# Performance work log

Hardware: AMD Instinct MI355X
Metric: run time of the kernel (lower is better)

Reference implementation:

```python
import jax, jax.numpy as jnp
import numpy as np

B, C, L = 2048, 9605, 8
ALPHA = 0.5        # self.alpha
ALPHA1 = 0.05      # margin
ALPHA2 = 2.0       # asymmetric scale when violated
ALPHA3 = 5.0       # logistic sharpness
ALPHA_OTHER = 0.3  # floor on top-k threshold
TOPK = 16          # x_sorted[15] -> 16th largest


def setup_inputs() -> dict:
    key = jax.random.key(0)
    k1, k2, k3, k4 = jax.random.split(key, 4)
    x = jax.random.normal(k1, (B, C), dtype=jnp.float32)
    # each class assigned to one of 5*L slots; slots < L are whitelist groups,
    # the rest are 'other' classes (like total_indices in the torch code)
    gid = jax.random.randint(k4, (C,), 0, 5 * L)
    gid = gid.at[:L].set(jnp.arange(L))  # guarantee every group is non-empty
    group_mask = gid[None, :] == jnp.arange(L)[:, None]  # [L, C] bool
    # sparse multi-label binarized targets (~14 positives/sample)
    y = (jax.random.uniform(k2, (B, C)) < 0.0015).astype(jnp.float32)
    y_neg = (jax.random.uniform(k3, (B, C)) < 0.0015).astype(jnp.float32)
    return {"x": x, "y": y, "y_neg": y_neg, "group_mask": group_mask}


def _rank_loss(x1, x2):
    # our_rank_loss: sigmoid(alpha3*(x2-x1+margin)), scaled by alpha2 when violated
    d = x2 - x1 + ALPHA1
    s = jax.nn.sigmoid(ALPHA3 * d)
    return jnp.where(d > 0, ALPHA2 * s, s)


def reference(x, y, y_neg, group_mask):
    xs = jax.nn.sigmoid(x)  # [B, C]
    # top_k_thres = max(16th-largest sigmoid score, alpha_other)
    thres = jnp.maximum(jax.lax.top_k(xs, TOPK)[0][:, TOPK - 1], ALPHA_OTHER)  # [B]
    maskf = group_mask.astype(xs.dtype)  # [L, C]
    neg_inf = jnp.array(-jnp.inf, xs.dtype)
    # per-sample max score inside each whitelist group: [B, L]
    group_max = jnp.max(jnp.where(group_mask[None, :, :], xs[:, None, :], neg_inf), axis=-1)
    # find_gt_whitelist: group is 'hit' if any positive target inside it
    gt = (y @ maskf.T) > 0        # [B, L]
    gt_neg = (y_neg @ maskf.T) > 0  # [B, L]
    has_gt = jnp.any(gt, axis=-1)    # [B]; False <=> sentinel len(all_labels)
    has_neg = jnp.any(gt_neg, axis=-1)
    # ---- case B: sample hits at least one whitelist group ----
    rl_correct = _rank_loss(group_max, thres[:, None])    # gt groups above thres
    rl_incorrect = _rank_loss(thres[:, None], group_max)  # non-gt groups below thres
    caseB = jnp.sum(jnp.where(gt, rl_correct, rl_incorrect), axis=-1)  # [B]
    # ---- case A: no whitelist group hit ----
    union = jnp.any(group_mask, axis=0)  # [C] union of all whitelist classes
    union_max = jnp.max(jnp.where(union[None, :], xs, neg_inf), axis=-1)  # [B]
    neg_max = jnp.max(jnp.where(gt_neg, group_max, neg_inf), axis=-1)
    neg_score = jnp.where(has_neg, neg_max, jnp.zeros((), xs.dtype))  # torch starts at 0
    caseA = (1.0 - ALPHA) * _rank_loss(thres, union_max) + ALPHA * _rank_loss(thres, neg_score)
    loss_rank_all = jnp.where(has_gt, caseB, caseA)  # [B]
    return jnp.mean(loss_rank_all)
```

## Files before the change

kernel.cpp:

```cpp
#include <hip/hip_runtime.h>
#include <math.h>

constexpr int B_ = 2048;
constexpr int C_ = 9605;
constexpr int L_ = 8;
constexpr int TOPK_ = 16;
constexpr int CAP_ = 512;
constexpr float T0_ = 2.0f;
constexpr int QW_ = 2404;
constexpr int NQ_ = (B_ * C_) / 4;

__device__ __forceinline__ float sigm(float v) { return 1.0f / (1.0f + expf(-v)); }

__device__ __forceinline__ float rank_loss(float x1, float x2) {
  float d = x2 - x1 + 0.05f;
  float s = 1.0f / (1.0f + expf(-5.0f * d));
  return (d > 0.0f) ? 2.0f * s : s;
}

__device__ __forceinline__ unsigned int fkey(float v) {
  unsigned int u = __float_as_uint(v);
  return u ^ ((u & 0x80000000u) ? 0xFFFFFFFFu : 0x80000000u);
}
__device__ __forceinline__ float fkeyinv(unsigned int k) {
  unsigned int u = (k & 0x80000000u) ? (k ^ 0x80000000u) : ~k;
  return __uint_as_float(u);
}

__global__ void build_code_kernel(const int* __restrict__ mask,
                                  unsigned char* __restrict__ code) {
  int c = blockIdx.x * 256 + threadIdx.x;
  if (c >= C_) return;
  unsigned char cd = 0xFF;
#pragma unroll
  for (int l = L_ - 1; l >= 0; --l)
    if (mask[l * C_ + c] != 0) cd = (unsigned char)l;
  code[c] = cd;
}

__global__ void pack_code_kernel(const unsigned char* __restrict__ code,
                                 unsigned int* __restrict__ codeq) {
  int k = blockIdx.x * 256 + threadIdx.x;
  int r = blockIdx.y;
  if (k >= QW_) return;
  unsigned int v = 0u;
#pragma unroll
  for (int e = 0; e < 4; ++e) {
    int c = r + 4 * k + e;
    unsigned int byte = (c < C_) ? (unsigned int)code[c] : 0xFFu;
    v |= byte << (8 * e);
  }
  codeq[r * QW_ + k] = v;
}

__global__ void __launch_bounds__(256) scan_pos_kernel(
    const float* __restrict__ y, const float* __restrict__ yn,
    const unsigned char* __restrict__ code,
    unsigned int* __restrict__ gtb, unsigned int* __restrict__ gnb) {
  const float* arr = (blockIdx.y == 0) ? y : yn;
  unsigned int* dst = (blockIdx.y == 0) ? gtb : gnb;
  const float4* a4 = reinterpret_cast<const float4*>(arr);
  const int S = gridDim.x * 256;
  int q = blockIdx.x * 256 + threadIdx.x;

  auto rare = [&](float v, int idx) {
    if (v > 0.0f) {
      int row = idx / C_;
      int col = idx - row * C_;
      unsigned char cd = code[col];
      if (cd < L_) atomicOr(&dst[row], 1u << cd);
    }
  };
  auto chk = [&](float4 v, int qq) {
    float m = fmaxf(fmaxf(v.x, v.y), fmaxf(v.z, v.w));
    if (m > 0.0f) {
      int base = qq << 2;
      rare(v.x, base); rare(v.y, base + 1); rare(v.z, base + 2); rare(v.w, base + 3);
    }
  };

  for (; q + 3 * S < NQ_; q += 4 * S) {
    float4 v0 = a4[q];
    float4 v1 = a4[q + S];
    float4 v2 = a4[q + 2 * S];
    float4 v3 = a4[q + 3 * S];
    chk(v0, q); chk(v1, q + S); chk(v2, q + 2 * S); chk(v3, q + 3 * S);
  }
  for (; q < NQ_; q += S) chk(a4[q], q);
}

__global__ void __launch_bounds__(256) row_loss_kernel(
    const float* __restrict__ x, const unsigned char* __restrict__ code,
    const unsigned int* __restrict__ codeq,
    const unsigned int* __restrict__ gtb_g, const unsigned int* __restrict__ gnb_g,
    float* __restrict__ loss) {
  __shared__ float cand[CAP_];
  __shared__ int cand_cnt;
  __shared__ float wgm[4][L_];
  __shared__ float s_x16;
  __shared__ int s_red;

  const int t = threadIdx.x;
  const int b = blockIdx.x;
  const float* xr = x + (size_t)b * C_;
  if (t == 0) cand_cnt = 0;

  float gm[L_];
#pragma unroll
  for (int l = 0; l < L_; ++l) gm[l] = -INFINITY;

  auto cappend = [&](float xv) {
    int p = atomicAdd(&cand_cnt, 1);
    if (p < CAP_) cand[p] = xv;
  };
  auto procq = [&](float4 xv, unsigned int cd4) {
    int c0 = (int)(cd4 & 0xFF), c1 = (int)((cd4 >> 8) & 0xFF);
    int c2 = (int)((cd4 >> 16) & 0xFF), c3 = (int)((cd4 >> 24) & 0xFF);
#pragma unroll
    for (int l = 0; l < L_; ++l) {
      float vl = (c0 == l) ? xv.x : -INFINITY;
      vl = (c1 == l) ? fmaxf(vl, xv.y) : vl;
      vl = (c2 == l) ? fmaxf(vl, xv.z) : vl;
      vl = (c3 == l) ? fmaxf(vl, xv.w) : vl;
      gm[l] = fmaxf(gm[l], vl);
    }
    if (xv.x > T0_) cappend(xv.x);
    if (xv.y > T0_) cappend(xv.y);
    if (xv.z > T0_) cappend(xv.z);
    if (xv.w > T0_) cappend(xv.w);
  };

  const int lead = (4 - (b & 3)) & 3;
  const int n4 = (C_ - lead) >> 2;
  const float4* x4 = reinterpret_cast<const float4*>(x) + (((size_t)b * C_ + lead) >> 2);
  const unsigned int* cq = codeq + lead * QW_;

  for (int kb = 0; kb < 2048; kb += 1024) {
    int k0 = kb + t, k1 = kb + 256 + t, k2 = kb + 512 + t, k3 = kb + 768 + t;
    float4 a0 = x4[k0];
    float4 a1 = x4[k1];
    float4 a2 = x4[k2];
    float4 a3 = x4[k3];
    unsigned int q0 = cq[k0], q1 = cq[k1], q2 = cq[k2], q3 = cq[k3];
    procq(a0, q0); procq(a1, q1); procq(a2, q2); procq(a3, q3);
  }
  for (int k = 2048 + t; k < n4; k += 256) procq(x4[k], cq[k]);

  if (t < lead) {
    float v = xr[t];
    int cd = (int)code[t];
#pragma unroll
    for (int l = 0; l < L_; ++l)
      if (cd == l) gm[l] = fmaxf(gm[l], v);
    if (v > T0_) cappend(v);
  }
  const int tstart = lead + (n4 << 2);
  if (t >= 4 && t < 4 + (C_ - tstart)) {
    int c = tstart + (t - 4);
    float v = xr[c];
    int cd = (int)code[c];
#pragma unroll
    for (int l = 0; l < L_; ++l)
      if (cd == l) gm[l] = fmaxf(gm[l], v);
    if (v > T0_) cappend(v);
  }

#pragma unroll
  for (int off = 32; off > 0; off >>= 1) {
#pragma unroll
    for (int l = 0; l < L_; ++l) gm[l] = fmaxf(gm[l], __shfl_xor(gm[l], off, 64));
  }
  if ((t & 63) == 0) {
    int w = t >> 6;
#pragma unroll
    for (int l = 0; l < L_; ++l) wgm[w][l] = gm[l];
  }
  __syncthreads();

  const int cnt = cand_cnt;
  const bool mainp = (cnt >= TOPK_) && (cnt <= CAP_);
  if (mainp) {
    if (t < 64) {
      unsigned int ku[CAP_ / 64];
#pragma unroll
      for (int k = 0; k < CAP_ / 64; ++k) {
        int idx = t + (k << 6);
        ku[k] = (idx < cnt) ? fkey(cand[idx]) : 0u;
      }
      unsigned int lo = 0u, hi = 0xFFFFFFFFu;
      for (int it = 0; it < 32 && lo < hi; ++it) {
        unsigned int mid = lo + ((hi - lo) >> 1) + 1u;
        int c16 = 0;
#pragma unroll
        for (int k = 0; k < CAP_ / 64; ++k) c16 += (ku[k] >= mid) ? 1 : 0;
#pragma unroll
        for (int off = 32; off > 0; off >>= 1) c16 += __shfl_xor(c16, off, 64);
        if (c16 >= TOPK_) lo = mid; else hi = mid - 1u;
      }
      if (t == 0) s_x16 = fkeyinv(lo);
    }
  } else {
    unsigned int lo = 0u, hi = 0xFFFFFFFFu;
    for (int it = 0; it < 32; ++it) {
      if (lo >= hi) break;
      unsigned int mid = lo + ((hi - lo) >> 1) + 1u;
      if (t == 0) s_red = 0;
      __syncthreads();
      int cl = 0;
      for (int c = t; c < C_; c += 256) cl += (fkey(xr[c]) >= mid) ? 1 : 0;
      atomicAdd(&s_red, cl);
      __syncthreads();
      int total = s_red;
      __syncthreads();
      if (total >= TOPK_) lo = mid; else hi = mid - 1u;
    }
    if (t == 0) s_x16 = fkeyinv(lo);
  }
  __syncthreads();

  if (t == 0) {
    float thres = fmaxf(sigm(s_x16), 0.3f);
    unsigned int gtbf = gtb_g[b];
    unsigned int gnbf = gnb_g[b];
    float caseB = 0.0f, unio = -INFINITY, negmax = -INFINITY;
#pragma unroll
    for (int l = 0; l < L_; ++l) {
      float gx = fmaxf(fmaxf(wgm[0][l], wgm[1][l]), fmaxf(wgm[2][l], wgm[3][l]));
      float g = sigm(gx);
      unio = fmaxf(unio, g);
      caseB += ((gtbf >> l) & 1u) ? rank_loss(g, thres) : rank_loss(thres, g);
      if ((gnbf >> l) & 1u) negmax = fmaxf(negmax, g);
    }
    float negscore = (gnbf != 0u) ? negmax : 0.0f;
    float caseA = 0.5f * rank_loss(thres, unio) + 0.5f * rank_loss(thres, negscore);
    loss[b] = (gtbf != 0u) ? caseB : caseA;
  }
}

__global__ void mean_kernel(const float* __restrict__ loss, float* __restrict__ out) {
  const int t = threadIdx.x;
  float s = 0.0f;
  for (int i = t; i < B_; i += 256) s += loss[i];
#pragma unroll
  for (int off = 32; off > 0; off >>= 1) s += __shfl_xor(s, off, 64);
  __shared__ float part[4];
  if ((t & 63) == 0) part[t >> 6] = s;
  __syncthreads();
  if (t == 0) out[0] = (part[0] + part[1] + part[2] + part[3]) * (1.0f / (float)B_);
}

extern "C" void kernel_launch(void* const* d_in, const int* in_sizes, int n_in,
                              void* d_out, int out_size, void* d_ws, size_t ws_size,
                              hipStream_t stream) {
  const float* x = (const float*)d_in[0];
  const float* y = (const float*)d_in[1];
  const float* yn = (const float*)d_in[2];
  const int* mask = (const int*)d_in[3];

  char* ws = (char*)d_ws;
  float* loss = (float*)ws;
  unsigned int* gtb = (unsigned int*)(ws + 8192);
  unsigned int* gnb = (unsigned int*)(ws + 16384);
  unsigned char* code = (unsigned char*)(ws + 24576);
  unsigned int* codeq = (unsigned int*)(ws + 24576 + 9632);

  hipMemsetAsync(gtb, 0, 2 * B_ * sizeof(unsigned int), stream);
  hipLaunchKernelGGL(build_code_kernel, dim3((C_ + 255) / 256), dim3(256), 0, stream,
                     mask, code);
  hipLaunchKernelGGL(pack_code_kernel, dim3((QW_ + 255) / 256, 4), dim3(256), 0, stream,
                     code, codeq);
  hipLaunchKernelGGL(scan_pos_kernel, dim3(2048, 2), dim3(256), 0, stream,
                     y, yn, code, gtb, gnb);
  hipLaunchKernelGGL(row_loss_kernel, dim3(B_), dim3(256), 0, stream,
                     x, code, codeq, gtb, gnb, loss);
  hipLaunchKernelGGL(mean_kernel, dim3(1), dim3(256), 0, stream,
                     loss, (float*)d_out);
}
```

Before: 262.1 us.

## Fuse positive-scan and row-loss into one interleaved-role kernel, move loss to finisher

Merges the y/y_neg positive scan and the per-row top-k/group-max work into a single launch whose blocks take one of three roles, so the memory-bound scan streams run concurrently with the x-row blocks instead of serializing. Because gtb/gnb are no longer complete when row blocks end, the rank-loss evaluation moves to a finish kernel that also does the mean via atomicAdd, replacing the separate mean kernel. This adds an intermediate buffer for group maxima and thresholds and an extra memset of the output.

```diff
diff --git a/kernel.cpp b/kernel.cpp
--- a/kernel.cpp
+++ b/kernel.cpp
@@ -9,6 +9,9 @@
 constexpr float T0_ = 2.0f;
 constexpr int QW_ = 2404;
 constexpr int NQ_ = (B_ * C_) / 4;
+constexpr int SCANB_ = 2048;
+
+typedef float vfloat4 __attribute__((ext_vector_type(4)));
 
 __device__ __forceinline__ float sigm(float v) { return 1.0f / (1.0f + expf(-v)); }
 
@@ -53,55 +56,56 @@
   codeq[r * QW_ + k] = v;
 }
 
-__global__ void __launch_bounds__(256) scan_pos_kernel(
-    const float* __restrict__ y, const float* __restrict__ yn,
-    const unsigned char* __restrict__ code,
-    unsigned int* __restrict__ gtb, unsigned int* __restrict__ gnb) {
-  const float* arr = (blockIdx.y == 0) ? y : yn;
-  unsigned int* dst = (blockIdx.y == 0) ? gtb : gnb;
-  const float4* a4 = reinterpret_cast<const float4*>(arr);
-  const int S = gridDim.x * 256;
-  int q = blockIdx.x * 256 + threadIdx.x;
-
-  auto rare = [&](float v, int idx) {
-    if (v > 0.0f) {
-      int row = idx / C_;
-      int col = idx - row * C_;
-      unsigned char cd = code[col];
-      if (cd < L_) atomicOr(&dst[row], 1u << cd);
-    }
-  };
-  auto chk = [&](float4 v, int qq) {
-    float m = fmaxf(fmaxf(v.x, v.y), fmaxf(v.z, v.w));
-    if (m > 0.0f) {
-      int base = qq << 2;
-      rare(v.x, base); rare(v.y, base + 1); rare(v.z, base + 2); rare(v.w, base + 3);
-    }
-  };
-
-  for (; q + 3 * S < NQ_; q += 4 * S) {
-    float4 v0 = a4[q];
-    float4 v1 = a4[q + S];
-    float4 v2 = a4[q + 2 * S];
-    float4 v3 = a4[q + 3 * S];
-    chk(v0, q); chk(v1, q + S); chk(v2, q + 2 * S); chk(v3, q + 3 * S);
-  }
-  for (; q < NQ_; q += S) chk(a4[q], q);
-}
-
-__global__ void __launch_bounds__(256) row_loss_kernel(
-    const float* __restrict__ x, const unsigned char* __restrict__ code,
+__global__ void __launch_bounds__(256) fused_main_kernel(
+    const float* __restrict__ x, const float* __restrict__ y,
+    const float* __restrict__ yn, const unsigned char* __restrict__ code,
     const unsigned int* __restrict__ codeq,
-    const unsigned int* __restrict__ gtb_g, const unsigned int* __restrict__ gnb_g,
-    float* __restrict__ loss) {
+    float* __restrict__ x16g, float* __restrict__ wgmg,
+    unsigned int* __restrict__ gtb_g, unsigned int* __restrict__ gnb_g) {
+  const int t = threadIdx.x;
+  const int role = blockIdx.x % 3;
+  const int sub = blockIdx.x / 3;
+
+  if (role != 0) {
+    const float* arr = (role == 1) ? y : yn;
+    unsigned int* dst = (role == 1) ? gtb_g : gnb_g;
+    const vfloat4* a4 = reinterpret_cast<const vfloat4*>(arr);
+    const int S = SCANB_ * 256;
+    int q = sub * 256 + t;
+
+    auto rare = [&](float v, int idx) {
+      if (v > 0.0f) {
+        int row = idx / C_;
+        int col = idx - row * C_;
+        unsigned char cd = code[col];
+        if (cd < L_) atomicOr(&dst[row], 1u << cd);
+      }
+    };
+    auto chk = [&](vfloat4 v, int qq) {
+      float m = fmaxf(fmaxf(v.x, v.y), fmaxf(v.z, v.w));
+      if (m > 0.0f) {
+        int base = qq << 2;
+        rare(v.x, base); rare(v.y, base + 1); rare(v.z, base + 2); rare(v.w, base + 3);
+      }
+    };
+    for (; q + 3 * S < NQ_; q += 4 * S) {
+      vfloat4 v0 = a4[q];
+      vfloat4 v1 = a4[q + S];
+      vfloat4 v2 = a4[q + 2 * S];
+      vfloat4 v3 = a4[q + 3 * S];
+      chk(v0, q); chk(v1, q + S); chk(v2, q + 2 * S); chk(v3, q + 3 * S);
+    }
+    for (; q < NQ_; q += S) chk(a4[q], q);
+    return;
+  }
+
   __shared__ float cand[CAP_];
   __shared__ int cand_cnt;
   __shared__ float wgm[4][L_];
   __shared__ float s_x16;
   __shared__ int s_red;
 
-  const int t = threadIdx.x;
-  const int b = blockIdx.x;
+  const int b = sub;
   const float* xr = x + (size_t)b * C_;
   if (t == 0) cand_cnt = 0;
 
@@ -113,7 +117,7 @@
     int p = atomicAdd(&cand_cnt, 1);
     if (p < CAP_) cand[p] = xv;
   };
-  auto procq = [&](float4 xv, unsigned int cd4) {
+  auto procq = [&](vfloat4 xv, unsigned int cd4) {
     int c0 = (int)(cd4 & 0xFF), c1 = (int)((cd4 >> 8) & 0xFF);
     int c2 = (int)((cd4 >> 16) & 0xFF), c3 = (int)((cd4 >> 24) & 0xFF);
 #pragma unroll
@@ -132,38 +136,31 @@
 
   const int lead = (4 - (b & 3)) & 3;
   const int n4 = (C_ - lead) >> 2;
-  const float4* x4 = reinterpret_cast<const float4*>(x) + (((size_t)b * C_ + lead) >> 2);
+  const vfloat4* x4 = reinterpret_cast<const vfloat4*>(x) + (((size_t)b * C_ + lead) >> 2);
   const unsigned int* cq = codeq + lead * QW_;
 
   for (int kb = 0; kb < 2048; kb += 1024) {
-    int k0 = kb + t, k1 = kb + 256 + t, k2 = kb + 512 + t, k3 = kb + 768 + t;
-    float4 a0 = x4[k0];
-    float4 a1 = x4[k1];
-    float4 a2 = x4[k2];
-    float4 a3 = x4[k3];
+    int k0 = kb + t, k1 = k0 + 256, k2 = k0 + 512, k3 = k0 + 768;
+    vfloat4 a0 = x4[k0];
+    vfloat4 a1 = x4[k1];
+    vfloat4 a2 = x4[k2];
+    vfloat4 a3 = x4[k3];
     unsigned int q0 = cq[k0], q1 = cq[k1], q2 = cq[k2], q3 = cq[k3];
     procq(a0, q0); procq(a1, q1); procq(a2, q2); procq(a3, q3);
   }
   for (int k = 2048 + t; k < n4; k += 256) procq(x4[k], cq[k]);
 
-  if (t < lead) {
-    float v = xr[t];
-    int cd = (int)code[t];
+  auto scalar_elem = [&](int c) {
+    float v = xr[c];
+    int cd = (int)code[c];
 #pragma unroll
     for (int l = 0; l < L_; ++l)
       if (cd == l) gm[l] = fmaxf(gm[l], v);
     if (v > T0_) cappend(v);
-  }
-  const int tstart = lead + (n4 << 2);
-  if (t >= 4 && t < 4 + (C_ - tstart)) {
-    int c = tstart + (t - 4);
-    float v = xr[c];
-    int cd = (int)code[c];
-#pragma unroll
-    for (int l = 0; l < L_; ++l)
-      if (cd == l) gm[l] = fmaxf(gm[l], v);
-    if (v > T0_) cappend(v);
-  }
+  };
+  if (t < lead) scalar_elem(t);
+  const int ts = lead + (n4 << 2);
+  if (t >= 64 && t < 64 + (C_ - ts)) scalar_elem(ts + (t - 64));
 
 #pragma unroll
   for (int off = 32; off > 0; off >>= 1) {
@@ -218,35 +215,43 @@
   }
   __syncthreads();
 
-  if (t == 0) {
-    float thres = fmaxf(sigm(s_x16), 0.3f);
-    unsigned int gtbf = gtb_g[b];
-    unsigned int gnbf = gnb_g[b];
+  if (t == 0) x16g[b] = s_x16;
+  if (t < L_) {
+    float gx = fmaxf(fmaxf(wgm[0][t], wgm[1][t]), fmaxf(wgm[2][t], wgm[3][t]));
+    wgmg[b * L_ + t] = gx;
+  }
+}
+
+__global__ void __launch_bounds__(256) finish_kernel(
+    const float* __restrict__ x16g, const float* __restrict__ wgmg,
+    const unsigned int* __restrict__ gtb_g, const unsigned int* __restrict__ gnb_g,
+    float* __restrict__ out) {
+  const int t = threadIdx.x;
+  const int r = blockIdx.x * 256 + t;
+  float lb = 0.0f;
+  if (r < B_) {
+    float thres = fmaxf(sigm(x16g[r]), 0.3f);
+    unsigned int gtbf = gtb_g[r];
+    unsigned int gnbf = gnb_g[r];
     float caseB = 0.0f, unio = -INFINITY, negmax = -INFINITY;
 #pragma unroll
     for (int l = 0; l < L_; ++l) {
-      float gx = fmaxf(fmaxf(wgm[0][l], wgm[1][l]), fmaxf(wgm[2][l], wgm[3][l]));
-      float g = sigm(gx);
+      float g = sigm(wgmg[r * L_ + l]);
       unio = fmaxf(unio, g);
       caseB += ((gtbf >> l) & 1u) ? rank_loss(g, thres) : rank_loss(thres, g);
       if ((gnbf >> l) & 1u) negmax = fmaxf(negmax, g);
     }
     float negscore = (gnbf != 0u) ? negmax : 0.0f;
     float caseA = 0.5f * rank_loss(thres, unio) + 0.5f * rank_loss(thres, negscore);
-    loss[b] = (gtbf != 0u) ? caseB : caseA;
-  }
-}
-
-__global__ void mean_kernel(const float* __restrict__ loss, float* __restrict__ out) {
-  const int t = threadIdx.x;
-  float s = 0.0f;
-  for (int i = t; i < B_; i += 256) s += loss[i];
-#pragma unroll
-  for (int off = 32; off > 0; off >>= 1) s += __shfl_xor(s, off, 64);
+    lb = (gtbf != 0u) ? caseB : caseA;
+  }
+#pragma unroll
+  for (int off = 32; off > 0; off >>= 1) lb += __shfl_xor(lb, off, 64);
   __shared__ float part[4];
-  if ((t & 63) == 0) part[t >> 6] = s;
+  if ((t & 63) == 0) part[t >> 6] = lb;
   __syncthreads();
-  if (t == 0) out[0] = (part[0] + part[1] + part[2] + part[3]) * (1.0f / (float)B_);
+  if (t == 0)
+    atomicAdd(out, (part[0] + part[1] + part[2] + part[3]) * (1.0f / (float)B_));
 }
 
 extern "C" void kernel_launch(void* const* d_in, const int* in_sizes, int n_in,
@@ -258,21 +263,22 @@
   const int* mask = (const int*)d_in[3];
 
   char* ws = (char*)d_ws;
-  float* loss = (float*)ws;
-  unsigned int* gtb = (unsigned int*)(ws + 8192);
-  unsigned int* gnb = (unsigned int*)(ws + 16384);
-  unsigned char* code = (unsigned char*)(ws + 24576);
-  unsigned int* codeq = (unsigned int*)(ws + 24576 + 9632);
-
-  hipMemsetAsync(gtb, 0, 2 * B_ * sizeof(unsigned int), stream);
+  float* x16g = (float*)ws;
+  float* wgmg = (float*)(ws + 8192);
+  unsigned int* gtb = (unsigned int*)(ws + 73728);
+  unsigned int* gnb = (unsigned int*)(ws + 81920);
+  unsigned char* code = (unsigned char*)(ws + 90112);
+  unsigned int* codeq = (unsigned int*)(ws + 90112 + 9632);
+
+  hipMemsetAsync(d_out, 0, sizeof(float), stream);
+  hipMemsetAsync(gtb, 0, B_ * sizeof(unsigned int), stream);
+  hipMemsetAsync(gnb, 0, B_ * sizeof(unsigned int), stream);
   hipLaunchKernelGGL(build_code_kernel, dim3((C_ + 255) / 256), dim3(256), 0, stream,
                      mask, code);
   hipLaunchKernelGGL(pack_code_kernel, dim3((QW_ + 255) / 256, 4), dim3(256), 0, stream,
                      code, codeq);
-  hipLaunchKernelGGL(scan_pos_kernel, dim3(2048, 2), dim3(256), 0, stream,
-                     y, yn, code, gtb, gnb);
-  hipLaunchKernelGGL(row_loss_kernel, dim3(B_), dim3(256), 0, stream,
-                     x, code, codeq, gtb, gnb, loss);
-  hipLaunchKernelGGL(mean_kernel, dim3(1), dim3(256), 0, stream,
-                     loss, (float*)d_out);
-}
+  hipLaunchKernelGGL(fused_main_kernel, dim3(3 * B_), dim3(256), 0, stream,
+                     x, y, yn, code, codeq, x16g, wgmg, gtb, gnb);
+  hipLaunchKernelGGL(finish_kernel, dim3((B_ + 255) / 256), dim3(256), 0, stream,
+                     x16g, wgmg, gtb, gnb, (float*)d_out);
+}
```

New measurement: 262.0 us. No clear change (-0.0%).
